# Performance work log

Hardware: AMD Instinct MI355X
Metric: run time of the kernel (lower is better)

## Reference

```python
import jax, jax.numpy as jnp
import numpy as np
from jax import lax

B, C_IN, IMG, P = 8, 320, 64, 2
H = W = IMG // P            # 32
N = H * W                   # 1024 tokens
DIM = 128 * P * P           # 512
DEPTH, HEADS, DH = 6, 8, 64
INNER = HEADS * DH          # 512
MLP = 512
EPS = 1e-5


def layernorm(x, g, b):
    mu = x.mean(-1, keepdims=True)
    var = ((x - mu) ** 2).mean(-1, keepdims=True)
    return (x - mu) * lax.rsqrt(var + EPS) * g + b


def conv3x3(x, w, b):
    y = lax.conv_general_dilated(x, w, (1, 1), 'SAME',
                                 dimension_numbers=('NCHW', 'OIHW', 'NCHW'))
    return y + b[None, :, None, None]


def posemb_sincos_2d(h, w, dim, temperature=10000.0):
    y, x = jnp.meshgrid(jnp.arange(h, dtype=jnp.float32),
                        jnp.arange(w, dtype=jnp.float32), indexing='ij')
    omega = jnp.arange(dim // 4, dtype=jnp.float32) / (dim // 4 - 1)
    omega = 1.0 / (temperature ** omega)
    y = y.reshape(-1)[:, None] * omega[None, :]
    x = x.reshape(-1)[:, None] * omega[None, :]
    return jnp.concatenate([jnp.sin(x), jnp.cos(x), jnp.sin(y), jnp.cos(y)], axis=1)


def prepare_attn_mask(mask):
    # attn mask allows position pairs where either row or col token is marked.
    f = 64 // H
    m = (mask == 1)
    r = m.reshape(-1, H, f, W, f).any(axis=(2, 4)).reshape(-1, N)  # [M, N] bool
    return r[:, :, None] | r[:, None, :]                            # [M, N, N]


def setup_inputs() -> dict:
    key = jax.random.key(0)
    ks = jax.random.split(key, 24)
    s = 0.02
    d = dict(
        img=jax.random.normal(ks[0], (B, C_IN, IMG, IMG), jnp.float32),
        mask=jax.random.randint(ks[1], (DEPTH * B, 64, 64), 0, 2, jnp.int32),
        conv1_w=jax.random.normal(ks[2], (128, C_IN, 3, 3), jnp.float32) * s,
        conv1_b=jnp.zeros((128,), jnp.float32),
        ln_p_g=jnp.ones((DIM,), jnp.float32), ln_p_b=jnp.zeros((DIM,), jnp.float32),
        proj_w=jax.random.normal(ks[3], (DIM, DIM), jnp.float32) * s,
        proj_b=jnp.zeros((DIM,), jnp.float32),
        ln_q_g=jnp.ones((DIM,), jnp.float32), ln_q_b=jnp.zeros((DIM,), jnp.float32),
        attn_ln_g=jnp.ones((DEPTH, DIM), jnp.float32),
        attn_ln_b=jnp.zeros((DEPTH, DIM), jnp.float32),
        wqkv=jax.random.normal(ks[4], (DEPTH, DIM, 3 * INNER), jnp.float32) * s,
        wo=jax.random.normal(ks[5], (DEPTH, INNER, DIM), jnp.float32) * s,
        ff_ln_g=jnp.ones((DEPTH, DIM), jnp.float32),
        ff_ln_b=jnp.zeros((DEPTH, DIM), jnp.float32),
        w1=jax.random.normal(ks[6], (DEPTH, DIM, MLP), jnp.float32) * s,
        b1=jnp.zeros((DEPTH, MLP), jnp.float32),
        w2=jax.random.normal(ks[7], (DEPTH, MLP, DIM), jnp.float32) * s,
        b2=jnp.zeros((DEPTH, DIM), jnp.float32),
        conv2_w=jax.random.normal(ks[8], (C_IN, 128, 3, 3), jnp.float32) * s,
        conv2_b=jnp.zeros((C_IN,), jnp.float32),
    )
    return d


def reference(img, mask, conv1_w, conv1_b, ln_p_g, ln_p_b, proj_w, proj_b,
              ln_q_g, ln_q_b, attn_ln_g, attn_ln_b, wqkv, wo,
              ff_ln_g, ff_ln_b, w1, b1, w2, b2, conv2_w, conv2_b):
    am = prepare_attn_mask(mask).reshape(DEPTH, B, N, N)  # per-layer masks

    # patch embed: conv -> rearrange 'b c (h p1) (w p2) -> b (h w) (p1 p2 c)'
    y = conv3x3(img, conv1_w, conv1_b)                           # [B,128,64,64]
    y = y.reshape(B, 128, H, P, W, P).transpose(0, 2, 4, 3, 5, 1)
    y = y.reshape(B, N, P * P * 128)                             # [B,N,512]
    x = layernorm(y, ln_p_g, ln_p_b) @ proj_w + proj_b
    x = layernorm(x, ln_q_g, ln_q_b)
    x = x + posemb_sincos_2d(H, W, DIM).astype(x.dtype)

    scale = DH ** -0.5
    for i in range(DEPTH):
        xn = layernorm(x, attn_ln_g[i], attn_ln_b[i])
        qkv = xn @ wqkv[i]                                       # [B,N,3*INNER]
        q, k, v = jnp.split(qkv, 3, axis=-1)
        q, k, v = (t.reshape(B, N, HEADS, DH).transpose(0, 2, 1, 3)
                   for t in (q, k, v))
        dots = jnp.einsum('bhid,bhjd->bhij', q, k) * scale
        min_val = lax.stop_gradient(dots.min())
        dots = jnp.where(am[i][:, None, :, :], dots, min_val)
        attn = jax.nn.softmax(dots, axis=-1)
        o = jnp.einsum('bhij,bhjd->bhid', attn, v)
        o = o.transpose(0, 2, 1, 3).reshape(B, N, INNER) @ wo[i]
        x = o + x
        h = layernorm(x, ff_ln_g[i], ff_ln_b[i]) @ w1[i] + b1[i]
        x = jax.nn.gelu(h, approximate=False) @ w2[i] + b2[i] + x

    # 'b (h w) (p1 p2 c) -> b c (h p1) (w p2)' then conv
    z = x.reshape(B, H, W, P, P, 128).transpose(0, 5, 1, 3, 2, 4)
    z = z.reshape(B, 128, IMG, IMG)
    return conv3x3(z, conv2_w, conv2_b)
```

## Files before the change

### kernel.cpp

```cpp
#include <hip/hip_runtime.h>
#include <hip/hip_bf16.h>
#include <math.h>

typedef __attribute__((ext_vector_type(8))) short short8;
typedef __attribute__((ext_vector_type(4))) float f32x4;
typedef unsigned short u16;
typedef unsigned int u32;
typedef unsigned long long u64;

#define DEV __device__ __forceinline__

DEV float bf2f(u16 u){ u32 x = ((u32)u)<<16; return __builtin_bit_cast(float, x); }
DEV u16 f2bf(float f){ u32 x = __builtin_bit_cast(u32, f); return (u16)((x + 0x7FFFu + ((x>>16)&1u))>>16); }
DEV f32x4 mfma16(short8 a, short8 b, f32x4 c){ return __builtin_amdgcn_mfma_f32_16x16x32_bf16(a,b,c,0,0,0); }
DEV void gload16(const void* g, void* l){
  __builtin_amdgcn_global_load_lds((const __attribute__((address_space(1))) void*)g,
                                   (__attribute__((address_space(3))) void*)l, 16, 0, 0);
}
DEV u32 fkey(float f){ u32 b = __builtin_bit_cast(u32, f); return (b & 0x80000000u) ? ~b : (b ^ 0x80000000u); }
DEV float funkey(u32 k){ u32 b = (k & 0x80000000u) ? (k ^ 0x80000000u) : ~k; return __builtin_bit_cast(float, b); }
DEV u32 cvtpk(float lo, float hi){ u32 d; asm("v_cvt_pk_bf16_f32 %0, %1, %2" : "=v"(d) : "v"(lo), "v"(hi)); return d; }

static constexpr size_t O_PROJW = 0;
static constexpr size_t O_QKVW  = O_PROJW + 524288;
static constexpr size_t O_WOW   = O_QKVW + 9437184;
static constexpr size_t O_W1W   = O_WOW + 3145728;
static constexpr size_t O_W2W   = O_W1W + 3145728;
static constexpr size_t O_C1W   = O_W2W + 3145728;
static constexpr size_t O_C2W   = O_C1W + 737280;
static constexpr size_t O_RA    = O_C2W + 737280;
static constexpr size_t O_RB    = O_RA + 22302720;
static constexpr size_t O_X     = O_RB + 25165824;
static constexpr size_t O_D     = O_X + 16777216;
static constexpr size_t O_F     = O_D + 8388608;
static constexpr size_t O_RM    = O_F + 8388608;
static constexpr size_t O_MIN   = O_RM + 49152;
static constexpr size_t O_RMB   = O_MIN + 256;
static constexpr size_t WS_NEED = O_RMB + 8192;

__global__ __launch_bounds__(256) void k_transpose_bf(const float* __restrict__ src, u16* __restrict__ dst, int K, int N){
  __shared__ float tile[32][33];
  const int k0 = blockIdx.x*32, n0 = blockIdx.y*32;
  src += (size_t)blockIdx.z*K*N; dst += (size_t)blockIdx.z*K*N;
  const int c = threadIdx.x & 31, r4 = threadIdx.x >> 5;
  for(int r=r4; r<32; r+=8) tile[r][c] = src[(size_t)(k0+r)*N + n0+c];
  __syncthreads();
  for(int r=r4; r<32; r+=8) dst[(size_t)(n0+r)*K + k0+c] = f2bf(tile[c][r]);
}

__global__ __launch_bounds__(256) void k_convw(const float* __restrict__ src, u16* __restrict__ dst, int OC, int IC){
  int idx = blockIdx.x*256 + threadIdx.x;
  int total = OC*IC*9;
  if(idx >= total) return;
  int oc = idx/(IC*9); int rem = idx - oc*IC*9; int tap = rem/IC; int ic = rem - tap*IC;
  dst[idx] = f2bf(src[(size_t)(oc*IC+ic)*9 + tap]);
}

__global__ __launch_bounds__(256) void k_pad_img(const float* __restrict__ img, u16* __restrict__ pcl){
  const int by = blockIdx.x; const int b = by>>6, y = by&63; const int c0 = blockIdx.y*64;
  __shared__ float t[64][65];
  const int tx = threadIdx.x & 63, tz = threadIdx.x >> 6;
  for(int ci=tz; ci<64; ci+=4) t[ci][tx] = img[(((size_t)b*320 + c0+ci)*64 + y)*64 + tx];
  __syncthreads();
  for(int x=tz; x<64; x+=4) pcl[(((size_t)b*66 + y+1)*66 + (x+1))*320 + c0 + tx] = f2bf(t[tx][x]);
}

__global__ __launch_bounds__(256) void k_pad_tok(const float* __restrict__ x, u16* __restrict__ pcl){
  int idx = blockIdx.x*256 + threadIdx.x;
  const int c = idx & 127; int r = idx >> 7; const int xx = r & 63; r >>= 6; const int yy = r & 63; const int b = r >> 6;
  const int n = (yy>>1)*32 + (xx>>1); const int f = (yy&1)*256 + (xx&1)*128 + c;
  pcl[(((size_t)b*66 + yy+1)*66 + xx+1)*128 + c] = f2bf(x[((size_t)b*1024 + n)*512 + f]);
}

__global__ __launch_bounds__(256) void k_rmask(const int* __restrict__ mask, unsigned char* __restrict__ rm,
                                               u64* __restrict__ rmbits){
  int idx = blockIdx.x*256 + threadIdx.x;
  const int m = idx >> 10, n = idx & 1023; const int h = n>>5, w = n&31;
  const int* mp = mask + ((size_t)m*64 + h*2)*64 + w*2;
  const int v = (mp[0]==1) | (mp[1]==1) | (mp[64]==1) | (mp[65]==1);
  rm[idx] = (unsigned char)v;
  const u64 bm = __ballot(v);
  if((threadIdx.x & 63) == 0) rmbits[idx>>6] = bm;
}

__global__ __launch_bounds__(256) void k_vt(const u16* __restrict__ v, u16* __restrict__ vt){
  const int nt = blockIdx.x, bh = blockIdx.y;
  __shared__ u16 t[64][72];
  const int tid = threadIdx.x;
  const int i = tid>>2, cq = tid&3;
  const u16* src = v + ((size_t)bh*1024 + nt*64 + i)*64 + cq*16;
  const short8 s0 = *(const short8*)src;
  const short8 s1 = *(const short8*)(src+8);
  #pragma unroll
  for(int e=0;e<8;e++){ t[cq*16+e][i] = (u16)s0[e]; t[cq*16+8+e][i] = (u16)s1[e]; }
  __syncthreads();
  short8 o0, o1;
  #pragma unroll
  for(int e=0;e<8;e++){ o0[e] = (short)t[i][cq*16+e]; o1[e] = (short)t[i][cq*16+8+e]; }
  u16* dst = vt + (size_t)bh*65536 + (size_t)i*1024 + nt*64 + cq*16;
  *(short8*)dst = o0;
  *(short8*)(dst+8) = o1;
}

__global__ __launch_bounds__(256) void k_ln_bf(const float* __restrict__ in, const float* __restrict__ gw,
                                               const float* __restrict__ bw, u16* __restrict__ out){
  const int tok = blockIdx.x*4 + (threadIdx.x>>6);
  const int lane = threadIdx.x & 63;
  const float* rp = in + (size_t)tok*512 + lane*8;
  const float4 a = *(const float4*)rp;
  const float4 b = *(const float4*)(rp+4);
  float s  = a.x+a.y+a.z+a.w + b.x+b.y+b.z+b.w;
  float sq = a.x*a.x+a.y*a.y+a.z*a.z+a.w*a.w + b.x*b.x+b.y*b.y+b.z*b.z+b.w*b.w;
  #pragma unroll
  for(int off=1; off<64; off<<=1){ s += __shfl_xor(s,off); sq += __shfl_xor(sq,off); }
  const float mu = s*(1.f/512.f);
  const float rs = rsqrtf(fmaxf(sq*(1.f/512.f) - mu*mu, 0.f) + 1e-5f);
  const float4 g0 = *(const float4*)(gw + lane*8);
  const float4 g1 = *(const float4*)(gw + lane*8 + 4);
  const float4 b0 = *(const float4*)(bw + lane*8);
  const float4 b1 = *(const float4*)(bw + lane*8 + 4);
  short8 o8;
  o8[0]=f2bf((a.x-mu)*rs*g0.x+b0.x); o8[1]=f2bf((a.y-mu)*rs*g0.y+b0.y);
  o8[2]=f2bf((a.z-mu)*rs*g0.z+b0.z); o8[3]=f2bf((a.w-mu)*rs*g0.w+b0.w);
  o8[4]=f2bf((b.x-mu)*rs*g1.x+b1.x); o8[5]=f2bf((b.y-mu)*rs*g1.y+b1.y);
  o8[6]=f2bf((b.z-mu)*rs*g1.z+b1.z); o8[7]=f2bf((b.w-mu)*rs*g1.w+b1.w);
  *(short8*)(out + (size_t)tok*512 + lane*8) = o8;
}

__global__ __launch_bounds__(256) void k_lnq_pos(const float* __restrict__ in, const float* __restrict__ gw,
                                                 const float* __restrict__ bw, float* __restrict__ out){
  const int tok = blockIdx.x*4 + (threadIdx.x>>6);
  const int lane = threadIdx.x & 63;
  const float* rp = in + (size_t)tok*512 + lane*8;
  const float4 a = *(const float4*)rp;
  const float4 b = *(const float4*)(rp+4);
  float s  = a.x+a.y+a.z+a.w + b.x+b.y+b.z+b.w;
  float sq = a.x*a.x+a.y*a.y+a.z*a.z+a.w*a.w + b.x*b.x+b.y*b.y+b.z*b.z+b.w*b.w;
  #pragma unroll
  for(int off=1; off<64; off<<=1){ s += __shfl_xor(s,off); sq += __shfl_xor(sq,off); }
  const float mu = s*(1.f/512.f);
  const float rs = rsqrtf(fmaxf(sq*(1.f/512.f) - mu*mu, 0.f) + 1e-5f);
  const int n = tok & 1023; const int yy = n>>5, xx = n&31;
  const int f0 = lane*8; const int sec = f0>>7;
  const float coord = (sec<2) ? (float)xx : (float)yy;
  const float vv[8] = {a.x,a.y,a.z,a.w,b.x,b.y,b.z,b.w};
  float ov[8];
  #pragma unroll
  for(int j=0;j<8;j++){
    const int f = f0+j; const int qq = f & 127;
    const float om = __expf(-(float)qq * (9.2103403719761836f/127.f));
    const float arg = coord * om;
    const float pe = (sec&1) ? __cosf(arg) : __sinf(arg);
    ov[j] = (vv[j]-mu)*rs*gw[f] + bw[f] + pe;
  }
  float* op = out + (size_t)tok*512 + f0;
  *(float4*)op = (float4){ov[0],ov[1],ov[2],ov[3]};
  *(float4*)(op+4) = (float4){ov[4],ov[5],ov[6],ov[7]};
}

template<int EPI, int CONVC>
__global__ __launch_bounds__(256, 4)
void k_gemm(const u16* __restrict__ A, const u16* __restrict__ Wt,
            const float* __restrict__ bias, void* __restrict__ outp,
            const float* __restrict__ resid, int M, int N, int Kd)
{
  __shared__ u16 Ald[2][4096];
  __shared__ u16 Bld[2][4096];
  const int tid = threadIdx.x, lane = tid & 63, wv = tid >> 6;
  const int lr = lane & 15, g = lane >> 4;
  const int m0 = blockIdx.x * 64, n0 = blockIdx.y * 64;
  const int wm = (wv >> 1) * 32, wn = (wv & 1) * 32;
  const int srow = tid >> 3;
  const int sc  = (tid & 7) ^ (srow & 7);
  int b0=0, yy0=0;
  if constexpr (CONVC != 0){ b0 = m0>>12; yy0 = (m0>>6)&63; }
  const u16* arow0p; const u16* arow1p;
  if constexpr (CONVC != 0){
    arow0p = A; arow1p = A;
  } else {
    arow0p = A + (size_t)(m0+srow)*Kd + sc*8;
    arow1p = A + (size_t)(m0+srow+32)*Kd + sc*8;
  }
  const u16* brow0p = Wt + (size_t)(n0+srow)*Kd + sc*8;
  const u16* brow1p = Wt + (size_t)(n0+srow+32)*Kd + sc*8;

  f32x4 acc[2][2];
  #pragma unroll
  for(int i=0;i<2;i++)
    #pragma unroll
    for(int j=0;j<2;j++) acc[i][j] = (f32x4){0.f,0.f,0.f,0.f};

  const int nIter = Kd >> 6;
  int cur = 0;

  auto stage = [&](int kt, int buf){
    const int k0 = kt << 6;
    const u16 *ga0, *ga1;
    if constexpr (CONVC != 0){
      const int tap = k0 / CONVC;
      const int ic0 = k0 - tap*CONVC;
      const int ky = tap/3, kx = tap - 3*(tap/3);
      const size_t rb0 = ((size_t)((b0*66 + yy0+ky)*66 + kx))*CONVC + ic0 + sc*8;
      ga0 = A + rb0 + (size_t)(srow)*CONVC;
      ga1 = A + rb0 + (size_t)(srow+32)*CONVC;
    } else {
      ga0 = arow0p + k0;
      ga1 = arow1p + k0;
    }
    gload16(ga0, &Ald[buf][tid*8]);
    gload16(ga1, &Ald[buf][2048 + tid*8]);
    gload16(brow0p + k0, &Bld[buf][tid*8]);
    gload16(brow1p + k0, &Bld[buf][2048 + tid*8]);
  };

  stage(0, 0);
  for(int kt=0; kt<nIter; ++kt){
    __syncthreads();
    if(kt+1 < nIter) stage(kt+1, cur^1);
    short8 af[2][2], bg[2][2];
    #pragma unroll
    for(int mi=0;mi<2;mi++)
      #pragma unroll
      for(int kk=0;kk<2;kk++){
        const int R = wm + mi*16 + lr;
        const int Rn = wn + mi*16 + lr;
        const int c = kk*4 + g;
        af[mi][kk] = *(const short8*)&Ald[cur][R*64 + ((c ^ (R&7))<<3)];
        bg[mi][kk] = *(const short8*)&Bld[cur][Rn*64 + ((c ^ (Rn&7))<<3)];
      }
    #pragma unroll
    for(int mi=0;mi<2;mi++)
      #pragma unroll
      for(int nj=0;nj<2;nj++)
        #pragma unroll
        for(int kk=0;kk<2;kk++)
          acc[mi][nj] = mfma16(af[mi][kk], bg[nj][kk], acc[mi][nj]);
    cur ^= 1;
  }

  #pragma unroll
  for(int mi=0;mi<2;mi++){
    #pragma unroll
    for(int nj=0;nj<2;nj++){
      #pragma unroll
      for(int r=0;r<4;r++){
        const int mrow = m0 + wm + mi*16 + g*4 + r;
        const int ncol = n0 + wn + nj*16 + lr;
        float val = acc[mi][nj][r];
        if constexpr (EPI==0 || EPI==3 || EPI==4 || EPI==5 || EPI==6)
          val += bias[ncol];
        if constexpr (EPI==0){
          ((float*)outp)[(size_t)mrow*512 + ncol] = val;
        } else if constexpr (EPI==1){
          const int sec = ncol >> 9, rem = ncol & 511;
          const int head = rem >> 6, d = rem & 63;
          const int b = mrow >> 10, t = mrow & 1023;
          ((u16*)outp)[(size_t)sec*4194304 + ((size_t)((b*8+head)*1024 + t))*64 + d] = f2bf(val);
        } else if constexpr (EPI==2 || EPI==4){
          const size_t idx = (size_t)mrow*512 + ncol;
          ((float*)outp)[idx] = resid[idx] + val;
        } else if constexpr (EPI==3){
          const float gl = 0.5f * val * (1.f + erff(val * 0.70710678118654752f));
          ((u16*)outp)[(size_t)mrow*512 + ncol] = f2bf(gl);
        } else if constexpr (EPI==5){
          const int b = mrow>>12; const int rr = mrow&4095; const int y = rr>>6; const int xx = rr&63;
          const size_t pidx = ((size_t)(b*1024 + (y>>1)*32 + (xx>>1)))*512 + (y&1)*256 + (xx&1)*128 + ncol;
          ((float*)outp)[pidx] = val;
        } else if constexpr (EPI==6){
          const int b = mrow>>12; const int rr = mrow&4095; const int y = rr>>6; const int xx = rr&63;
          ((float*)outp)[(((size_t)(b*320 + ncol))*64 + y)*64 + xx] = val;
        }
      }
    }
  }
}

__global__ __launch_bounds__(256, 3)
void k_gemmW(const u16* __restrict__ A, const u16* __restrict__ Wt,
             void* __restrict__ outp, int Kd)
{
  __shared__ u16 Ald[2][8192];
  __shared__ u16 Bld[2][4096];
  const int tid = threadIdx.x, lane = tid & 63, wv = tid >> 6;
  const int lr = lane & 15, g = lane >> 4;
  const int m0 = blockIdx.x * 128, n0 = blockIdx.y * 64;
  const int wm = wv * 32;
  const int srow = tid >> 3;
  const int sc  = (tid & 7) ^ (srow & 7);
  const u16* ar[4];
  #pragma unroll
  for(int j=0;j<4;j++) ar[j] = A + (size_t)(m0+srow+32*j)*Kd + sc*8;
  const u16* br0 = Wt + (size_t)(n0+srow)*Kd + sc*8;
  const u16* br1 = Wt + (size_t)(n0+srow+32)*Kd + sc*8;

  f32x4 acc[2][4];
  #pragma unroll
  for(int i=0;i<2;i++)
    #pragma unroll
    for(int j=0;j<4;j++) acc[i][j] = (f32x4){0.f,0.f,0.f,0.f};

  const int nIter = Kd >> 6;
  int cur = 0;
  auto stage = [&](int kt, int buf){
    const int k0 = kt << 6;
    #pragma unroll
    for(int j=0;j<4;j++) gload16(ar[j] + k0, &Ald[buf][j*2048 + tid*8]);
    gload16(br0 + k0, &Bld[buf][tid*8]);
    gload16(br1 + k0, &Bld[buf][2048 + tid*8]);
  };

  stage(0, 0);
  for(int kt=0; kt<nIter; ++kt){
    __syncthreads();
    if(kt+1 < nIter) stage(kt+1, cur^1);
    short8 af[2][2], bg[4][2];
    #pragma unroll
    for(int mi=0;mi<2;mi++)
      #pragma unroll
      for(int kk=0;kk<2;kk++){
        const int R = wm + mi*16 + lr;
        const int c = kk*4 + g;
        af[mi][kk] = *(const short8*)&Ald[cur][R*64 + ((c ^ (R&7))<<3)];
      }
    #pragma unroll
    for(int nj=0;nj<4;nj++)
      #pragma unroll
      for(int kk=0;kk<2;kk++){
        const int Rn = nj*16 + lr;
        const int c = kk*4 + g;
        bg[nj][kk] = *(const short8*)&Bld[cur][Rn*64 + ((c ^ (Rn&7))<<3)];
      }
    #pragma unroll
    for(int mi=0;mi<2;mi++)
      #pragma unroll
      for(int nj=0;nj<4;nj++)
        #pragma unroll
        for(int kk=0;kk<2;kk++)
          acc[mi][nj] = mfma16(af[mi][kk], bg[nj][kk], acc[mi][nj]);
    cur ^= 1;
  }

  #pragma unroll
  for(int mi=0;mi<2;mi++){
    #pragma unroll
    for(int nj=0;nj<4;nj++){
      #pragma unroll
      for(int r=0;r<4;r++){
        const int mrow = m0 + wm + mi*16 + g*4 + r;
        const int ncol = n0 + nj*16 + lr;
        const int sec = ncol >> 9, rem = ncol & 511;
        const int head = rem >> 6, d = rem & 63;
        const int b = mrow >> 10, t = mrow & 1023;
        ((u16*)outp)[(size_t)sec*4194304 + ((size_t)((b*8+head)*1024 + t))*64 + d] = f2bf(acc[mi][nj][r]);
      }
    }
  }
}

__global__ __launch_bounds__(256, 4)
void k_attn_minmax(const u16* __restrict__ q, const u16* __restrict__ k, u32* __restrict__ keys, int layer){
  const int id = blockIdx.x;
  const int qt = (id>>3)&15;
  const int bh = ((id&7)<<3) | (id>>7);
  __shared__ u16 Kld[2][4096];
  __shared__ float redn[4], redx[4];
  const int tid = threadIdx.x, lane = tid & 63, wv = tid >> 6;
  const int lr = lane & 15, g = lane >> 4;
  const u16* qp = q + ((size_t)bh*1024 + qt*64 + wv*16 + lr)*64;
  const short8 qa0 = *(const short8*)(qp + g*8);
  const short8 qa1 = *(const short8*)(qp + 32 + g*8);
  const u16* kbase = k + (size_t)bh*65536;
  const int srow = tid>>3, scs = lane&7;
  const int scg = scs ^ (srow&7);
  const int srow2 = srow + 32;
  const int scg2 = scs ^ (srow2&7);
  float mn = 3.0e38f, mx = -3.0e38f;
  gload16(kbase + (size_t)srow*64 + scg*8, &Kld[0][wv*512]);
  gload16(kbase + (size_t)srow2*64 + scg2*8, &Kld[0][2048 + wv*512]);
  int cur = 0;
  for(int jt=0; jt<16; ++jt){
    __syncthreads();
    if(jt < 15){
      const int j1 = (jt+1)*64;
      gload16(kbase + (size_t)(j1+srow)*64 + scg*8, &Kld[cur^1][wv*512]);
      gload16(kbase + (size_t)(j1+srow2)*64 + scg2*8, &Kld[cur^1][2048 + wv*512]);
    }
    #pragma unroll
    for(int c=0;c<4;c++){
      const int rr = c*16 + lr;
      const short8 kb0 = *(const short8*)&Kld[cur][rr*64 + ((g ^ (rr&7))<<3)];
      const short8 kb1 = *(const short8*)&Kld[cur][rr*64 + (((g+4) ^ (rr&7))<<3)];
      f32x4 s4 = (f32x4){0.f,0.f,0.f,0.f};
      __builtin_amdgcn_s_setprio(1);
      s4 = mfma16(qa0, kb0, s4);
      s4 = mfma16(qa1, kb1, s4);
      __builtin_amdgcn_s_setprio(0);
      mn = fminf(mn, fminf(fminf(s4[0],s4[1]), fminf(s4[2],s4[3])));
      mx = fmaxf(mx, fmaxf(fmaxf(s4[0],s4[1]), fmaxf(s4[2],s4[3])));
    }
    cur ^= 1;
  }
  mn *= 0.125f; mx *= 0.125f;
  #pragma unroll
  for(int off=32; off; off>>=1){
    mn = fminf(mn, __shfl_down(mn, off));
    mx = fmaxf(mx, __shfl_down(mx, off));
  }
  if(lane==0){ redn[wv] = mn; redx[wv] = mx; }
  __syncthreads();
  if(tid==0){
    atomicMin(keys + layer,     fkey(fminf(fminf(redn[0],redn[1]), fminf(redn[2],redn[3]))));
    atomicMax(keys + 8 + layer, fkey(fmaxf(fmaxf(redx[0],redx[1]), fmaxf(redx[2],redx[3]))));
  }
}

__global__ __launch_bounds__(256, 4)
void k_attn(const u16* __restrict__ q, const u16* __restrict__ k, const u16* __restrict__ vt,
            const u64* __restrict__ rmbits, const u32* __restrict__ keys,
            u16* __restrict__ o, int layer){
  const int id = blockIdx.x;
  const int qt = (id>>3)&15;
  const int bh = ((id&7)<<3) | (id>>7);
  const int b = bh>>3, h = bh&7;
  __shared__ u16 Kld[2][4096];
  __shared__ u16 Vtld[2][4096];
  __shared__ u32 Pld[4][512];
  const int tid = threadIdx.x, lane = tid & 63, wv = tid >> 6;
  const int lr = lane & 15, g = lane >> 4;
  const int L7 = lr & 7;
  const u16* qp = q + ((size_t)bh*1024 + qt*64 + wv*16 + lr)*64;
  const short8 qa0 = *(const short8*)(qp + g*8);
  const short8 qa1 = *(const short8*)(qp + 32 + g*8);
  const float L2E = 1.44269504088896f;
  const float SC = 0.125f * L2E;
  float mnv = funkey(keys[layer]);
  float mxv = funkey(keys[8+layer]);
  if(!(mnv >= -1e38f && mnv <= 1e38f)) mnv = 0.f;
  if(!(mxv >= -1e38f && mxv <= 1e38f)) mxv = 0.f;
  const float ME   = mxv * L2E;
  const float minM = fmaxf(mnv*L2E - ME, -120.f);
  const u32* cbp = (const u32*)(rmbits + (size_t)(layer*8 + b)*16);
  const u32 qbitw = cbp[qt*2 + ((wv*16+lr)>>5)];
  const u32 rfill = ((qbitw >> ((wv*16+lr)&31)) & 1u) ? 0xFu : 0u;
  u32* Pw = &Pld[wv][0];
  u32 wslot[4][2];
  #pragma unroll
  for(int c=0;c<4;c++){
    const int blk = c*2 + (g>>1);
    wslot[c][0] = lr*32 + ((blk ^ L7)<<2) + (g&1)*2;
    wslot[c][1] = wslot[c][0] + 1;
  }
  const u32 ra0 = lr*32 + ((g ^ L7)<<2);
  const u32 ra1 = lr*32 + (((4+g) ^ L7)<<2);

  float lsum = 0.f;
  f32x4 accd[4];
  #pragma unroll
  for(int d=0;d<4;d++) accd[d] = (f32x4){0.f,0.f,0.f,0.f};
  const u16* kbase = k + (size_t)bh*65536;
  const u16* vtbase = vt + (size_t)bh*65536;
  const int srow = tid>>3, scs = lane&7;
  const int scg = scs ^ (srow&7);
  const int srow2 = srow + 32;
  const int scg2 = scs ^ (srow2&7);
  gload16(kbase + (size_t)srow*64 + scg*8, &Kld[0][wv*512]);
  gload16(kbase + (size_t)srow2*64 + scg2*8, &Kld[0][2048 + wv*512]);
  gload16(vtbase + (size_t)srow*1024 + scg*8, &Vtld[0][wv*512]);
  gload16(vtbase + (size_t)srow2*1024 + scg2*8, &Vtld[0][2048 + wv*512]);
  int cur = 0;
  for(int jt=0; jt<16; ++jt){
    __syncthreads();
    if(jt < 15){
      const int j1 = (jt+1)*64;
      gload16(kbase + (size_t)(j1+srow)*64 + scg*8, &Kld[cur^1][wv*512]);
      gload16(kbase + (size_t)(j1+srow2)*64 + scg2*8, &Kld[cur^1][2048 + wv*512]);
      gload16(vtbase + (size_t)srow*1024 + j1 + scg*8, &Vtld[cur^1][wv*512]);
      gload16(vtbase + (size_t)srow2*1024 + j1 + scg2*8, &Vtld[cur^1][2048 + wv*512]);
    }
    const u32 cb_lo = cbp[jt*2], cb_hi = cbp[jt*2+1];
    #pragma unroll
    for(int c=0;c<4;c++){
      const int rr = c*16 + lr;
      const short8 kb0 = *(const short8*)&Kld[cur][rr*64 + ((g ^ (rr&7))<<3)];
      const short8 kb1 = *(const short8*)&Kld[cur][rr*64 + (((g+4) ^ (rr&7))<<3)];
      f32x4 s4 = (f32x4){0.f,0.f,0.f,0.f};
      __builtin_amdgcn_s_setprio(1);
      s4 = mfma16(kb0, qa0, s4);
      s4 = mfma16(kb1, qa1, s4);
      __builtin_amdgcn_s_setprio(0);
      const u32 cw = (((c<2) ? cb_lo : cb_hi) >> ((c&1)*16 + g*4)) | rfill;
      float e[4];
      #pragma unroll
      for(int r=0;r<4;r++){
        float sv = fmaxf(fmaf(s4[r], SC, -ME), -120.f);
        const float vl = ((cw >> r) & 1u) ? sv : minM;
        e[r] = exp2f(vl);
        lsum += e[r];
      }
      Pw[wslot[c][0]] = cvtpk(e[0], e[1]);
      Pw[wslot[c][1]] = cvtpk(e[2], e[3]);
    }
    asm volatile("s_waitcnt lgkmcnt(0)" ::: "memory");
    __builtin_amdgcn_sched_barrier(0);
    const short8 pa0 = *(const short8*)&Pw[ra0];
    const short8 pa1 = *(const short8*)&Pw[ra1];
    #pragma unroll
    for(int d=0;d<4;d++){
      const int rr = d*16 + lr;
      const short8 vb0 = *(const short8*)&Vtld[cur][rr*64 + ((g ^ (rr&7))<<3)];
      const short8 vb1 = *(const short8*)&Vtld[cur][rr*64 + (((g+4) ^ (rr&7))<<3)];
      __builtin_amdgcn_s_setprio(1);
      accd[d] = mfma16(pa0, vb0, accd[d]);
      accd[d] = mfma16(pa1, vb1, accd[d]);
      __builtin_amdgcn_s_setprio(0);
    }
    cur ^= 1;
  }
  lsum += __shfl_xor(lsum, 16);
  lsum += __shfl_xor(lsum, 32);
  float inv[4];
  #pragma unroll
  for(int r=0;r<4;r++) inv[r] = 1.f / __shfl(lsum, g*4 + r);
  #pragma unroll
  for(int d=0;d<4;d++)
    #pragma unroll
    for(int r=0;r<4;r++){
      const int qrow = qt*64 + wv*16 + g*4 + r;
      o[((size_t)b*1024 + qrow)*512 + h*64 + d*16 + lr] = f2bf(accd[d][r] * inv[r]);
    }
}

extern "C" void kernel_launch(void* const* d_in, const int* in_sizes, int n_in,
                              void* d_out, int out_size, void* d_ws, size_t ws_size,
                              hipStream_t stream)
{
  const float* img     = (const float*)d_in[0];
  const int*   mask    = (const int*)d_in[1];
  const float* conv1_w = (const float*)d_in[2];
  const float* conv1_b = (const float*)d_in[3];
  const float* ln_p_g  = (const float*)d_in[4];
  const float* ln_p_b  = (const float*)d_in[5];
  const float* proj_w  = (const float*)d_in[6];
  const float* proj_b  = (const float*)d_in[7];
  const float* ln_q_g  = (const float*)d_in[8];
  const float* ln_q_b  = (const float*)d_in[9];
  const float* attn_ln_g = (const float*)d_in[10];
  const float* attn_ln_b = (const float*)d_in[11];
  const float* wqkv    = (const float*)d_in[12];
  const float* wo      = (const float*)d_in[13];
  const float* ff_ln_g = (const float*)d_in[14];
  const float* ff_ln_b = (const float*)d_in[15];
  const float* w1      = (const float*)d_in[16];
  const float* b1      = (const float*)d_in[17];
  const float* w2      = (const float*)d_in[18];
  const float* b2      = (const float*)d_in[19];
  const float* conv2_w = (const float*)d_in[20];
  const float* conv2_b = (const float*)d_in[21];

  if(ws_size < WS_NEED) return;
  char* ws = (char*)d_ws;
  u16* projWt = (u16*)(ws + O_PROJW);
  u16* qkvWt  = (u16*)(ws + O_QKVW);
  u16* woWt   = (u16*)(ws + O_WOW);
  u16* w1Wt   = (u16*)(ws + O_W1W);
  u16* w2Wt   = (u16*)(ws + O_W2W);
  u16* c1Wt   = (u16*)(ws + O_C1W);
  u16* c2Wt   = (u16*)(ws + O_C2W);
  u16* pcl    = (u16*)(ws + O_RA);
  float* tmpf = (float*)(ws + O_RA);
  u16* vtb    = (u16*)(ws + O_RA);
  float* patches = (float*)(ws + O_RB);
  u16* qkvb   = (u16*)(ws + O_RB);
  float* xbuf = (float*)(ws + O_X);
  u16* xnbf   = (u16*)(ws + O_D);
  u16* obf    = (u16*)(ws + O_F);
  unsigned char* rmb = (unsigned char*)(ws + O_RM);
  u32* minbuf = (u32*)(ws + O_MIN);
  u64* rmbits = (u64*)(ws + O_RMB);

  hipMemsetAsync(ws + O_MIN, 0xFF, 32, stream);
  hipMemsetAsync(ws + O_MIN + 32, 0, 32, stream);
  hipMemsetAsync(ws + O_RA, 0, 22302720, stream);

  k_transpose_bf<<<dim3(16,16,1),256,0,stream>>>(proj_w, projWt, 512, 512);
  k_transpose_bf<<<dim3(16,48,6),256,0,stream>>>(wqkv,   qkvWt,  512, 1536);
  k_transpose_bf<<<dim3(16,16,6),256,0,stream>>>(wo,     woWt,   512, 512);
  k_transpose_bf<<<dim3(16,16,6),256,0,stream>>>(w1,     w1Wt,   512, 512);
  k_transpose_bf<<<dim3(16,16,6),256,0,stream>>>(w2,     w2Wt,   512, 512);
  k_convw<<<1440,256,0,stream>>>(conv1_w, c1Wt, 128, 320);
  k_convw<<<1440,256,0,stream>>>(conv2_w, c2Wt, 320, 128);
  k_rmask<<<192,256,0,stream>>>(mask, rmb, rmbits);

  k_pad_img<<<dim3(512,5),256,0,stream>>>(img, pcl);
  k_gemm<5,320><<<dim3(512,2),256,0,stream>>>(pcl, c1Wt, conv1_b, patches, nullptr, 32768, 128, 2880);
  k_ln_bf<<<2048,256,0,stream>>>(patches, ln_p_g, ln_p_b, xnbf);
  k_gemm<0,0><<<dim3(128,8),256,0,stream>>>(xnbf, projWt, proj_b, tmpf, nullptr, 8192, 512, 512);
  k_lnq_pos<<<2048,256,0,stream>>>(tmpf, ln_q_g, ln_q_b, xbuf);

  const u16* qb = qkvb;
  const u16* kb = qkvb + 4194304;
  const u16* vb = qkvb + 8388608;
  for(int i=0;i<6;i++){
    k_ln_bf<<<2048,256,0,stream>>>(xbuf, attn_ln_g + i*512, attn_ln_b + i*512, xnbf);
    k_gemmW<<<dim3(64,24),256,0,stream>>>(xnbf, qkvWt + (size_t)i*1536*512, qkvb, 512);
    k_vt<<<dim3(16,64),256,0,stream>>>(vb, vtb);
    k_attn_minmax<<<1024,256,0,stream>>>(qb, kb, minbuf, i);
    k_attn<<<1024,256,0,stream>>>(qb, kb, vtb, rmbits, minbuf, obf, i);
    k_gemm<2,0><<<dim3(128,8),256,0,stream>>>(obf, woWt + (size_t)i*512*512, nullptr, xbuf, xbuf, 8192, 512, 512);
    k_ln_bf<<<2048,256,0,stream>>>(xbuf, ff_ln_g + i*512, ff_ln_b + i*512, xnbf);
    k_gemm<3,0><<<dim3(128,8),256,0,stream>>>(xnbf, w1Wt + (size_t)i*512*512, b1 + i*512, obf, nullptr, 8192, 512, 512);
    k_gemm<4,0><<<dim3(128,8),256,0,stream>>>(obf, w2Wt + (size_t)i*512*512, b2 + i*512, xbuf, xbuf, 8192, 512, 512);
  }

  hipMemsetAsync(ws + O_RA, 0, 8921088, stream);
  k_pad_tok<<<16384,256,0,stream>>>(xbuf, pcl);
  k_gemm<6,128><<<dim3(512,5),256,0,stream>>>(pcl, c2Wt, conv2_b, d_out, nullptr, 32768, 320, 1152);
}
```

Baseline: 1.031 ms.

## Fuse V transpose into QKV GEMM epilogue and process two query tiles per attention block

The QKV GEMM now writes V directly in transposed layout through an LDS staging tile for the V column blocks, which removes the separate k_vt kernel and its extra global round trip. Both the min/max pass and the attention kernel now handle 128 query rows per block (two 64-row halves sharing each K/V tile load), so the grid shrinks from 1024 to 512 blocks and K/V reuse doubles. This costs more registers and LDS in the attention kernel (occupancy hint lowered to 3) and fewer blocks to spread across CUs. The unused byte-mask output is also dropped.

```diff
diff --git a/kernel.cpp b/kernel.cpp
--- a/kernel.cpp
+++ b/kernel.cpp
@@ -72,34 +72,13 @@
   pcl[(((size_t)b*66 + yy+1)*66 + xx+1)*128 + c] = f2bf(x[((size_t)b*1024 + n)*512 + f]);
 }
 
-__global__ __launch_bounds__(256) void k_rmask(const int* __restrict__ mask, unsigned char* __restrict__ rm,
-                                               u64* __restrict__ rmbits){
+__global__ __launch_bounds__(256) void k_rmask(const int* __restrict__ mask, u64* __restrict__ rmbits){
   int idx = blockIdx.x*256 + threadIdx.x;
   const int m = idx >> 10, n = idx & 1023; const int h = n>>5, w = n&31;
   const int* mp = mask + ((size_t)m*64 + h*2)*64 + w*2;
   const int v = (mp[0]==1) | (mp[1]==1) | (mp[64]==1) | (mp[65]==1);
-  rm[idx] = (unsigned char)v;
   const u64 bm = __ballot(v);
   if((threadIdx.x & 63) == 0) rmbits[idx>>6] = bm;
-}
-
-__global__ __launch_bounds__(256) void k_vt(const u16* __restrict__ v, u16* __restrict__ vt){
-  const int nt = blockIdx.x, bh = blockIdx.y;
-  __shared__ u16 t[64][72];
-  const int tid = threadIdx.x;
-  const int i = tid>>2, cq = tid&3;
-  const u16* src = v + ((size_t)bh*1024 + nt*64 + i)*64 + cq*16;
-  const short8 s0 = *(const short8*)src;
-  const short8 s1 = *(const short8*)(src+8);
-  #pragma unroll
-  for(int e=0;e<8;e++){ t[cq*16+e][i] = (u16)s0[e]; t[cq*16+8+e][i] = (u16)s1[e]; }
-  __syncthreads();
-  short8 o0, o1;
-  #pragma unroll
-  for(int e=0;e<8;e++){ o0[e] = (short)t[i][cq*16+e]; o1[e] = (short)t[i][cq*16+8+e]; }
-  u16* dst = vt + (size_t)bh*65536 + (size_t)i*1024 + nt*64 + cq*16;
-  *(short8*)dst = o0;
-  *(short8*)(dst+8) = o1;
 }
 
 __global__ __launch_bounds__(256) void k_ln_bf(const float* __restrict__ in, const float* __restrict__ gw,
@@ -251,11 +230,6 @@
           val += bias[ncol];
         if constexpr (EPI==0){
           ((float*)outp)[(size_t)mrow*512 + ncol] = val;
-        } else if constexpr (EPI==1){
-          const int sec = ncol >> 9, rem = ncol & 511;
-          const int head = rem >> 6, d = rem & 63;
-          const int b = mrow >> 10, t = mrow & 1023;
-          ((u16*)outp)[(size_t)sec*4194304 + ((size_t)((b*8+head)*1024 + t))*64 + d] = f2bf(val);
         } else if constexpr (EPI==2 || EPI==4){
           const size_t idx = (size_t)mrow*512 + ncol;
           ((float*)outp)[idx] = resid[idx] + val;
@@ -277,7 +251,7 @@
 
 __global__ __launch_bounds__(256, 3)
 void k_gemmW(const u16* __restrict__ A, const u16* __restrict__ Wt,
-             void* __restrict__ outp, int Kd)
+             void* __restrict__ outp, u16* __restrict__ vt, int Kd)
 {
   __shared__ u16 Ald[2][8192];
   __shared__ u16 Bld[2][4096];
@@ -340,35 +314,64 @@
     cur ^= 1;
   }
 
-  #pragma unroll
-  for(int mi=0;mi<2;mi++){
-    #pragma unroll
-    for(int nj=0;nj<4;nj++){
-      #pragma unroll
-      for(int r=0;r<4;r++){
-        const int mrow = m0 + wm + mi*16 + g*4 + r;
-        const int ncol = n0 + nj*16 + lr;
-        const int sec = ncol >> 9, rem = ncol & 511;
-        const int head = rem >> 6, d = rem & 63;
-        const int b = mrow >> 10, t = mrow & 1023;
-        ((u16*)outp)[(size_t)sec*4194304 + ((size_t)((b*8+head)*1024 + t))*64 + d] = f2bf(acc[mi][nj][r]);
+  if(n0 < 1024){
+    #pragma unroll
+    for(int mi=0;mi<2;mi++){
+      #pragma unroll
+      for(int nj=0;nj<4;nj++){
+        #pragma unroll
+        for(int r=0;r<4;r++){
+          const int mrow = m0 + wm + mi*16 + g*4 + r;
+          const int ncol = n0 + nj*16 + lr;
+          const int sec = ncol >> 9, rem = ncol & 511;
+          const int head = rem >> 6, d = rem & 63;
+          const int b = mrow >> 10, t = mrow & 1023;
+          ((u16*)outp)[(size_t)sec*4194304 + ((size_t)((b*8+head)*1024 + t))*64 + d] = f2bf(acc[mi][nj][r]);
+        }
       }
     }
+  } else {
+    const int head = (n0 - 1024) >> 6;
+    const int b = m0 >> 10;
+    const int t0 = m0 & 1023;
+    const int bh = b*8 + head;
+    __syncthreads();
+    u16* Vt = (u16*)Ald;
+    #pragma unroll
+    for(int mi=0;mi<2;mi++)
+      #pragma unroll
+      for(int nj=0;nj<4;nj++)
+        #pragma unroll
+        for(int r=0;r<4;r++){
+          const int lt = wm + mi*16 + g*4 + r;
+          const int d  = nj*16 + lr;
+          Vt[d*136 + lt] = f2bf(acc[mi][nj][r]);
+        }
+    __syncthreads();
+    const int d = tid >> 2, qd = tid & 3;
+    u16* dst = vt + (size_t)bh*65536 + (size_t)d*1024 + t0 + qd*32;
+    const u16* srcl = &Vt[d*136 + qd*32];
+    #pragma unroll
+    for(int e4=0;e4<4;e4++)
+      *(short8*)(dst + e4*8) = *(const short8*)(srcl + e4*8);
   }
 }
 
 __global__ __launch_bounds__(256, 4)
 void k_attn_minmax(const u16* __restrict__ q, const u16* __restrict__ k, u32* __restrict__ keys, int layer){
   const int id = blockIdx.x;
-  const int qt = (id>>3)&15;
-  const int bh = ((id&7)<<3) | (id>>7);
+  const int qt = (id>>3)&7;
+  const int bh = ((id&7)<<3) | (id>>6);
   __shared__ u16 Kld[2][4096];
   __shared__ float redn[4], redx[4];
   const int tid = threadIdx.x, lane = tid & 63, wv = tid >> 6;
   const int lr = lane & 15, g = lane >> 4;
-  const u16* qp = q + ((size_t)bh*1024 + qt*64 + wv*16 + lr)*64;
-  const short8 qa0 = *(const short8*)(qp + g*8);
-  const short8 qa1 = *(const short8*)(qp + 32 + g*8);
+  const u16* qp0 = q + ((size_t)bh*1024 + qt*128 + wv*16 + lr)*64;
+  const u16* qp1 = qp0 + 64*64;
+  const short8 qa00 = *(const short8*)(qp0 + g*8);
+  const short8 qa01 = *(const short8*)(qp0 + 32 + g*8);
+  const short8 qa10 = *(const short8*)(qp1 + g*8);
+  const short8 qa11 = *(const short8*)(qp1 + 32 + g*8);
   const u16* kbase = k + (size_t)bh*65536;
   const int srow = tid>>3, scs = lane&7;
   const int scg = scs ^ (srow&7);
@@ -390,13 +393,18 @@
       const int rr = c*16 + lr;
       const short8 kb0 = *(const short8*)&Kld[cur][rr*64 + ((g ^ (rr&7))<<3)];
       const short8 kb1 = *(const short8*)&Kld[cur][rr*64 + (((g+4) ^ (rr&7))<<3)];
-      f32x4 s4 = (f32x4){0.f,0.f,0.f,0.f};
+      f32x4 sa = (f32x4){0.f,0.f,0.f,0.f};
+      f32x4 sb = (f32x4){0.f,0.f,0.f,0.f};
       __builtin_amdgcn_s_setprio(1);
-      s4 = mfma16(qa0, kb0, s4);
-      s4 = mfma16(qa1, kb1, s4);
+      sa = mfma16(qa00, kb0, sa);
+      sa = mfma16(qa01, kb1, sa);
+      sb = mfma16(qa10, kb0, sb);
+      sb = mfma16(qa11, kb1, sb);
       __builtin_amdgcn_s_setprio(0);
-      mn = fminf(mn, fminf(fminf(s4[0],s4[1]), fminf(s4[2],s4[3])));
-      mx = fmaxf(mx, fmaxf(fmaxf(s4[0],s4[1]), fmaxf(s4[2],s4[3])));
+      mn = fminf(mn, fminf(fminf(sa[0],sa[1]), fminf(sa[2],sa[3])));
+      mx = fmaxf(mx, fmaxf(fmaxf(sa[0],sa[1]), fmaxf(sa[2],sa[3])));
+      mn = fminf(mn, fminf(fminf(sb[0],sb[1]), fminf(sb[2],sb[3])));
+      mx = fmaxf(mx, fmaxf(fmaxf(sb[0],sb[1]), fmaxf(sb[2],sb[3])));
     }
     cur ^= 1;
   }
@@ -414,23 +422,26 @@
   }
 }
 
-__global__ __launch_bounds__(256, 4)
+__global__ __launch_bounds__(256, 3)
 void k_attn(const u16* __restrict__ q, const u16* __restrict__ k, const u16* __restrict__ vt,
             const u64* __restrict__ rmbits, const u32* __restrict__ keys,
             u16* __restrict__ o, int layer){
   const int id = blockIdx.x;
-  const int qt = (id>>3)&15;
-  const int bh = ((id&7)<<3) | (id>>7);
+  const int qt = (id>>3)&7;
+  const int bh = ((id&7)<<3) | (id>>6);
   const int b = bh>>3, h = bh&7;
   __shared__ u16 Kld[2][4096];
   __shared__ u16 Vtld[2][4096];
-  __shared__ u32 Pld[4][512];
+  __shared__ u32 Pld[4][1024];
   const int tid = threadIdx.x, lane = tid & 63, wv = tid >> 6;
   const int lr = lane & 15, g = lane >> 4;
   const int L7 = lr & 7;
-  const u16* qp = q + ((size_t)bh*1024 + qt*64 + wv*16 + lr)*64;
-  const short8 qa0 = *(const short8*)(qp + g*8);
-  const short8 qa1 = *(const short8*)(qp + 32 + g*8);
+  const u16* qp0 = q + ((size_t)bh*1024 + qt*128 + wv*16 + lr)*64;
+  const u16* qp1 = qp0 + 64*64;
+  const short8 qa00 = *(const short8*)(qp0 + g*8);
+  const short8 qa01 = *(const short8*)(qp0 + 32 + g*8);
+  const short8 qa10 = *(const short8*)(qp1 + g*8);
+  const short8 qa11 = *(const short8*)(qp1 + 32 + g*8);
   const float L2E = 1.44269504088896f;
   const float SC = 0.125f * L2E;
   float mnv = funkey(keys[layer]);
@@ -440,8 +451,10 @@
   const float ME   = mxv * L2E;
   const float minM = fmaxf(mnv*L2E - ME, -120.f);
   const u32* cbp = (const u32*)(rmbits + (size_t)(layer*8 + b)*16);
-  const u32 qbitw = cbp[qt*2 + ((wv*16+lr)>>5)];
-  const u32 rfill = ((qbitw >> ((wv*16+lr)&31)) & 1u) ? 0xFu : 0u;
+  const int rowi0 = qt*128 + wv*16 + lr;
+  const int rowi1 = rowi0 + 64;
+  const u32 rf0 = ((cbp[rowi0>>5] >> (rowi0&31)) & 1u) ? 0xFu : 0u;
+  const u32 rf1 = ((cbp[rowi1>>5] >> (rowi1&31)) & 1u) ? 0xFu : 0u;
   u32* Pw = &Pld[wv][0];
   u32 wslot[4][2];
   #pragma unroll
@@ -453,10 +466,10 @@
   const u32 ra0 = lr*32 + ((g ^ L7)<<2);
   const u32 ra1 = lr*32 + (((4+g) ^ L7)<<2);
 
-  float lsum = 0.f;
-  f32x4 accd[4];
-  #pragma unroll
-  for(int d=0;d<4;d++) accd[d] = (f32x4){0.f,0.f,0.f,0.f};
+  float ls0 = 0.f, ls1 = 0.f;
+  f32x4 acc0[4], acc1[4];
+  #pragma unroll
+  for(int d=0;d<4;d++){ acc0[d] = (f32x4){0.f,0.f,0.f,0.f}; acc1[d] = (f32x4){0.f,0.f,0.f,0.f}; }
   const u16* kbase = k + (size_t)bh*65536;
   const u16* vtbase = vt + (size_t)bh*65536;
   const int srow = tid>>3, scs = lane&7;
@@ -483,50 +496,63 @@
       const int rr = c*16 + lr;
       const short8 kb0 = *(const short8*)&Kld[cur][rr*64 + ((g ^ (rr&7))<<3)];
       const short8 kb1 = *(const short8*)&Kld[cur][rr*64 + (((g+4) ^ (rr&7))<<3)];
-      f32x4 s4 = (f32x4){0.f,0.f,0.f,0.f};
+      f32x4 sa = (f32x4){0.f,0.f,0.f,0.f};
+      f32x4 sb = (f32x4){0.f,0.f,0.f,0.f};
       __builtin_amdgcn_s_setprio(1);
-      s4 = mfma16(kb0, qa0, s4);
-      s4 = mfma16(kb1, qa1, s4);
+      sa = mfma16(kb0, qa00, sa);
+      sa = mfma16(kb1, qa01, sa);
+      sb = mfma16(kb0, qa10, sb);
+      sb = mfma16(kb1, qa11, sb);
       __builtin_amdgcn_s_setprio(0);
-      const u32 cw = (((c<2) ? cb_lo : cb_hi) >> ((c&1)*16 + g*4)) | rfill;
-      float e[4];
+      const u32 base = (((c<2) ? cb_lo : cb_hi) >> ((c&1)*16 + g*4));
+      const u32 cw0 = base | rf0;
+      const u32 cw1 = base | rf1;
+      float e0[4], e1[4];
       #pragma unroll
       for(int r=0;r<4;r++){
-        float sv = fmaxf(fmaf(s4[r], SC, -ME), -120.f);
-        const float vl = ((cw >> r) & 1u) ? sv : minM;
-        e[r] = exp2f(vl);
-        lsum += e[r];
+        float sv0 = fmaxf(fmaf(sa[r], SC, -ME), -120.f);
+        float sv1 = fmaxf(fmaf(sb[r], SC, -ME), -120.f);
+        e0[r] = exp2f(((cw0 >> r) & 1u) ? sv0 : minM);
+        e1[r] = exp2f(((cw1 >> r) & 1u) ? sv1 : minM);
+        ls0 += e0[r]; ls1 += e1[r];
       }
-      Pw[wslot[c][0]] = cvtpk(e[0], e[1]);
-      Pw[wslot[c][1]] = cvtpk(e[2], e[3]);
+      Pw[wslot[c][0]]       = cvtpk(e0[0], e0[1]);
+      Pw[wslot[c][1]]       = cvtpk(e0[2], e0[3]);
+      Pw[512 + wslot[c][0]] = cvtpk(e1[0], e1[1]);
+      Pw[512 + wslot[c][1]] = cvtpk(e1[2], e1[3]);
     }
     asm volatile("s_waitcnt lgkmcnt(0)" ::: "memory");
     __builtin_amdgcn_sched_barrier(0);
-    const short8 pa0 = *(const short8*)&Pw[ra0];
-    const short8 pa1 = *(const short8*)&Pw[ra1];
+    const short8 pa00 = *(const short8*)&Pw[ra0];
+    const short8 pa01 = *(const short8*)&Pw[ra1];
+    const short8 pa10 = *(const short8*)&Pw[512 + ra0];
+    const short8 pa11 = *(const short8*)&Pw[512 + ra1];
     #pragma unroll
     for(int d=0;d<4;d++){
       const int rr = d*16 + lr;
       const short8 vb0 = *(const short8*)&Vtld[cur][rr*64 + ((g ^ (rr&7))<<3)];
       const short8 vb1 = *(const short8*)&Vtld[cur][rr*64 + (((g+4) ^ (rr&7))<<3)];
       __builtin_amdgcn_s_setprio(1);
-      accd[d] = mfma16(pa0, vb0, accd[d]);
-      accd[d] = mfma16(pa1, vb1, accd[d]);
+      acc0[d] = mfma16(pa00, vb0, acc0[d]);
+      acc0[d] = mfma16(pa01, vb1, acc0[d]);
+      acc1[d] = mfma16(pa10, vb0, acc1[d]);
+      acc1[d] = mfma16(pa11, vb1, acc1[d]);
       __builtin_amdgcn_s_setprio(0);
     }
     cur ^= 1;
   }
-  lsum += __shfl_xor(lsum, 16);
-  lsum += __shfl_xor(lsum, 32);
-  float inv[4];
-  #pragma unroll
-  for(int r=0;r<4;r++) inv[r] = 1.f / __shfl(lsum, g*4 + r);
+  ls0 += __shfl_xor(ls0, 16); ls0 += __shfl_xor(ls0, 32);
+  ls1 += __shfl_xor(ls1, 16); ls1 += __shfl_xor(ls1, 32);
+  float inv0[4], inv1[4];
+  #pragma unroll
+  for(int r=0;r<4;r++){ inv0[r] = 1.f / __shfl(ls0, g*4 + r); inv1[r] = 1.f / __shfl(ls1, g*4 + r); }
   #pragma unroll
   for(int d=0;d<4;d++)
     #pragma unroll
     for(int r=0;r<4;r++){
-      const int qrow = qt*64 + wv*16 + g*4 + r;
-      o[((size_t)b*1024 + qrow)*512 + h*64 + d*16 + lr] = f2bf(accd[d][r] * inv[r]);
+      const int qr0 = qt*128 + wv*16 + g*4 + r;
+      o[((size_t)b*1024 + qr0)*512 + h*64 + d*16 + lr]        = f2bf(acc0[d][r] * inv0[r]);
+      o[((size_t)b*1024 + qr0 + 64)*512 + h*64 + d*16 + lr]   = f2bf(acc1[d][r] * inv1[r]);
     }
 }
 
@@ -574,7 +600,6 @@
   float* xbuf = (float*)(ws + O_X);
   u16* xnbf   = (u16*)(ws + O_D);
   u16* obf    = (u16*)(ws + O_F);
-  unsigned char* rmb = (unsigned char*)(ws + O_RM);
   u32* minbuf = (u32*)(ws + O_MIN);
   u64* rmbits = (u64*)(ws + O_RMB);
 
@@ -589,7 +614,7 @@
   k_transpose_bf<<<dim3(16,16,6),256,0,stream>>>(w2,     w2Wt,   512, 512);
   k_convw<<<1440,256,0,stream>>>(conv1_w, c1Wt, 128, 320);
   k_convw<<<1440,256,0,stream>>>(conv2_w, c2Wt, 320, 128);
-  k_rmask<<<192,256,0,stream>>>(mask, rmb, rmbits);
+  k_rmask<<<192,256,0,stream>>>(mask, rmbits);
 
   k_pad_img<<<dim3(512,5),256,0,stream>>>(img, pcl);
   k_gemm<5,320><<<dim3(512,2),256,0,stream>>>(pcl, c1Wt, conv1_b, patches, nullptr, 32768, 128, 2880);
@@ -599,13 +624,11 @@
 
   const u16* qb = qkvb;
   const u16* kb = qkvb + 4194304;
-  const u16* vb = qkvb + 8388608;
   for(int i=0;i<6;i++){
     k_ln_bf<<<2048,256,0,stream>>>(xbuf, attn_ln_g + i*512, attn_ln_b + i*512, xnbf);
-    k_gemmW<<<dim3(64,24),256,0,stream>>>(xnbf, qkvWt + (size_t)i*1536*512, qkvb, 512);
-    k_vt<<<dim3(16,64),256,0,stream>>>(vb, vtb);
-    k_attn_minmax<<<1024,256,0,stream>>>(qb, kb, minbuf, i);
-    k_attn<<<1024,256,0,stream>>>(qb, kb, vtb, rmbits, minbuf, obf, i);
+    k_gemmW<<<dim3(64,24),256,0,stream>>>(xnbf, qkvWt + (size_t)i*1536*512, qkvb, vtb, 512);
+    k_attn_minmax<<<512,256,0,stream>>>(qb, kb, minbuf, i);
+    k_attn<<<512,256,0,stream>>>(qb, kb, vtb, rmbits, minbuf, obf, i);
     k_gemm<2,0><<<dim3(128,8),256,0,stream>>>(obf, woWt + (size_t)i*512*512, nullptr, xbuf, xbuf, 8192, 512, 512);
     k_ln_bf<<<2048,256,0,stream>>>(xbuf, ff_ln_g + i*512, ff_ln_b + i*512, xnbf);
     k_gemm<3,0><<<dim3(128,8),256,0,stream>>>(xnbf, w1Wt + (size_t)i*512*512, b1 + i*512, obf, nullptr, 8192, 512, 512);
```

Result: faster. 961.5 us (-6.7%).
